# Kernel optimization log

Hardware: AMD Instinct MI355X
Metric: run time of the kernel (lower is better)

Reference implementation:

```python
import jax, jax.numpy as jnp
import numpy as np

N_NODES = 100000
N_EDGES = 1600000

def gcn_conv(x, src, dst, W, b, n):
    # symmetric GCN normalization with self-loops already included in src/dst
    deg = jax.ops.segment_sum(jnp.ones_like(src, dtype=x.dtype), dst, num_segments=n)
    dinv = jnp.where(deg > 0, jax.lax.rsqrt(deg), 0.0)
    norm = dinv[src] * dinv[dst]            # [E]
    h = x @ W                                # [n, out]
    msg = h[src] * norm[:, None]             # gather + scale, [E, out]
    out = jax.ops.segment_sum(msg, dst, num_segments=n)  # scatter-add
    return out + b

def setup_inputs() -> dict:
    key = jax.random.key(0)
    k1, k2, k3, k4 = jax.random.split(key, 4)
    x = jax.random.normal(k1, (N_NODES, 768), dtype=jnp.float32)
    edge_index = jax.random.randint(k2, (2, N_EDGES), 0, N_NODES, dtype=jnp.int64)
    W1 = jax.random.normal(k3, (768, 64), dtype=jnp.float32) * (1.0 / np.sqrt(768))
    b1 = jnp.zeros((64,), dtype=jnp.float32)
    W2 = jax.random.normal(k4, (64, 32), dtype=jnp.float32) * (1.0 / np.sqrt(64))
    b2 = jnp.zeros((32,), dtype=jnp.float32)
    return {"x": x, "edge_index": edge_index, "W1": W1, "b1": b1, "W2": W2, "b2": b2}

def reference(x, edge_index, W1, b1, W2, b2):
    n = x.shape[0]
    loop = jnp.arange(n, dtype=edge_index.dtype)
    src = jnp.concatenate([edge_index[0], loop])
    dst = jnp.concatenate([edge_index[1], loop])
    h = jax.nn.relu(gcn_conv(x, src, dst, W1, b1, n))
    # F.dropout with training=False -> identity (eval mode)
    out = gcn_conv(h, src, dst, W2, b2, n)
    return out
```

## Files before the change

### kernel.cpp

```cpp
#include <hip/hip_runtime.h>


constexpr int C1 = 64;
constexpr int C2 = 32;
constexpr int K1 = 768;
constexpr int SCAN_BS = 256;
constexpr int SCAN_ELEMS = 2048;

__global__ void detect_k(const int* __restrict__ ei32, int* flag, int n_words) {
    __shared__ int any_nz;
    if (threadIdx.x == 0) any_nz = 0;
    __syncthreads();
    int w = 2 * threadIdx.x + 1;
    if (w < n_words && ei32[w] != 0) atomicOr(&any_nz, 1);
    __syncthreads();
    if (threadIdx.x == 0) *flag = (any_nz == 0) ? 1 : 0;
}

__device__ __forceinline__ int load_idx(const void* ei, size_t pos, int m64) {
    if (m64) return (int)((const long long*)ei)[pos];
    return ((const int*)ei)[pos];
}

__global__ void zero_k(int* p, int n) {
    int i = blockIdx.x * 256 + threadIdx.x;
    if (i < n) p[i] = 0;
}

__global__ void cnt_k(const void* __restrict__ ei, const int* __restrict__ flag,
                      int* cnt, int E) {
    int e = blockIdx.x * 256 + threadIdx.x;
    if (e >= E) return;
    int m64 = *flag;
    int d = load_idx(ei, (size_t)E + e, m64);
    atomicAdd(&cnt[d], 1);
}

__global__ void dinv_k(const int* __restrict__ cnt, float* dinv, int n) {
    int i = blockIdx.x * 256 + threadIdx.x;
    if (i < n) dinv[i] = rsqrtf(1.0f + (float)cnt[i]);
}

__global__ void scan1_k(const int* __restrict__ cnt, int* partials, int n) {
    __shared__ int s[SCAN_BS];
    int base = blockIdx.x * SCAN_ELEMS;
    int t = threadIdx.x;
    int sum = 0;
    #pragma unroll
    for (int i = 0; i < 8; ++i) {
        int idx = base + t * 8 + i;
        if (idx < n) sum += cnt[idx];
    }
    s[t] = sum;
    __syncthreads();
    for (int off = 128; off > 0; off >>= 1) {
        if (t < off) s[t] += s[t + off];
        __syncthreads();
    }
    if (t == 0) partials[blockIdx.x] = s[0];
}

__global__ void scan2_k(int* partials, int* total_out, int nb) {
    __shared__ int s[256];
    int t = threadIdx.x;
    int v = (t < nb) ? partials[t] : 0;
    s[t] = v;
    __syncthreads();
    for (int off = 1; off < 256; off <<= 1) {
        int add = (t >= off) ? s[t - off] : 0;
        __syncthreads();
        s[t] += add;
        __syncthreads();
    }
    if (t < nb) partials[t] = s[t] - v;
    if (t == 0) *total_out = s[255];
}

__global__ void scan3_k(const int* __restrict__ cnt, const int* __restrict__ partials,
                        int* offsets, int* cursor, int n) {
    __shared__ int s[SCAN_BS];
    int base = blockIdx.x * SCAN_ELEMS;
    int t = threadIdx.x;
    int local[8];
    int sum = 0;
    #pragma unroll
    for (int i = 0; i < 8; ++i) {
        int idx = base + t * 8 + i;
        int v = (idx < n) ? cnt[idx] : 0;
        local[i] = sum;
        sum += v;
    }
    int mine = sum;
    s[t] = sum;
    __syncthreads();
    for (int off = 1; off < 256; off <<= 1) {
        int add = (t >= off) ? s[t - off] : 0;
        __syncthreads();
        s[t] += add;
        __syncthreads();
    }
    int texcl = s[t] - mine;
    int boff = partials[blockIdx.x];
    #pragma unroll
    for (int i = 0; i < 8; ++i) {
        int idx = base + t * 8 + i;
        if (idx < n) {
            int o = boff + texcl + local[i];
            offsets[idx] = o;
            cursor[idx] = o;
        }
    }
}

__global__ void fill_k(const void* __restrict__ ei, const int* __restrict__ flag,
                       int* cursor, int* adj, int E) {
    int e = blockIdx.x * 256 + threadIdx.x;
    if (e >= E) return;
    int m64 = *flag;
    int s = load_idx(ei, e, m64);
    int d = load_idx(ei, (size_t)E + e, m64);
    int pos = atomicAdd(&cursor[d], 1);
    adj[pos] = s;
}

__global__ __launch_bounds__(256) void gemm1_k(const float* __restrict__ x,
                                               const float* __restrict__ W,
                                               const float* __restrict__ dinv,
                                               float* __restrict__ g1, int n) {
    __shared__ float As[32][64];
    __shared__ float Bs[32][64];
    const int tid = threadIdx.x;
    const int block_row = blockIdx.x * 64;
    const int tr = tid >> 4;
    const int tc = tid & 15;

    float acc[4][4] = {};

    for (int k0 = 0; k0 < K1; k0 += 32) {
        #pragma unroll
        for (int i = 0; i < 2; ++i) {
            int f = tid + i * 256;
            int row = f >> 3;
            int k4 = (f & 7) << 2;
            int grow = block_row + row;
            float4 v = make_float4(0.f, 0.f, 0.f, 0.f);
            if (grow < n) v = *(const float4*)(x + (size_t)grow * K1 + k0 + k4);
            As[k4 + 0][row] = v.x; As[k4 + 1][row] = v.y;
            As[k4 + 2][row] = v.z; As[k4 + 3][row] = v.w;
        }
        #pragma unroll
        for (int i = 0; i < 2; ++i) {
            int f = tid + i * 256;
            int kr = f >> 4;
            int c4 = (f & 15) << 2;
            *(float4*)&Bs[kr][c4] = *(const float4*)(W + (size_t)(k0 + kr) * C1 + c4);
        }
        __syncthreads();
        #pragma unroll
        for (int kk = 0; kk < 32; ++kk) {
            float4 a = *(float4*)&As[kk][tr << 2];
            float4 b = *(float4*)&Bs[kk][tc << 2];
            acc[0][0] += a.x * b.x; acc[0][1] += a.x * b.y; acc[0][2] += a.x * b.z; acc[0][3] += a.x * b.w;
            acc[1][0] += a.y * b.x; acc[1][1] += a.y * b.y; acc[1][2] += a.y * b.z; acc[1][3] += a.y * b.w;
            acc[2][0] += a.z * b.x; acc[2][1] += a.z * b.y; acc[2][2] += a.z * b.z; acc[2][3] += a.z * b.w;
            acc[3][0] += a.w * b.x; acc[3][1] += a.w * b.y; acc[3][2] += a.w * b.z; acc[3][3] += a.w * b.w;
        }
        __syncthreads();
    }
    #pragma unroll
    for (int i = 0; i < 4; ++i) {
        int grow = block_row + (tr << 2) + i;
        if (grow < n) {
            float dv = dinv[grow];
            *(float4*)(g1 + (size_t)grow * C1 + (tc << 2)) =
                make_float4(acc[i][0] * dv, acc[i][1] * dv, acc[i][2] * dv, acc[i][3] * dv);
        }
    }
}

__global__ __launch_bounds__(256) void gather1_k(const int* __restrict__ offsets,
                                                 const int* __restrict__ adj,
                                                 const float* __restrict__ dinv,
                                                 const float* __restrict__ g1,
                                                 const float* __restrict__ b1,
                                                 const float* __restrict__ W2,
                                                 float* __restrict__ g2, int n) {
    __shared__ float sW[C1 * C2];
    __shared__ float srow[4][C1];
    const int tid = threadIdx.x;
    for (int i = tid; i < C1 * C2; i += 256) sW[i] = W2[i];

    const int wid = tid >> 6;
    const int c = tid & 63;
    const int v = blockIdx.x * 4 + wid;

    float r = 0.f;
    float dv = 0.f;
    if (v < n) {
        dv = dinv[v];
        int start = offsets[v], end = offsets[v + 1];
        float acc = g1[(size_t)v * C1 + c];
        int j = start;
        for (; j + 4 <= end; j += 4) {
            int s0 = adj[j], s1 = adj[j + 1], s2 = adj[j + 2], s3 = adj[j + 3];
            float a0 = g1[(size_t)s0 * C1 + c];
            float a1 = g1[(size_t)s1 * C1 + c];
            float a2 = g1[(size_t)s2 * C1 + c];
            float a3 = g1[(size_t)s3 * C1 + c];
            acc += (a0 + a1) + (a2 + a3);
        }
        for (; j < end; ++j) acc += g1[(size_t)adj[j] * C1 + c];
        r = fmaxf(b1[c] + dv * acc, 0.f);
    }
    srow[wid][c] = r;
    __syncthreads();

    if (v < n && c < C2) {
        float acc = 0.f;
        #pragma unroll
        for (int k = 0; k < C1; ++k) acc += srow[wid][k] * sW[k * C2 + c];
        g2[(size_t)v * C2 + c] = dv * acc;
    }
}

__global__ __launch_bounds__(256) void gather2_k(const int* __restrict__ offsets,
                                                 const int* __restrict__ adj,
                                                 const float* __restrict__ dinv,
                                                 const float* __restrict__ g2,
                                                 const float* __restrict__ b2,
                                                 float* __restrict__ out, int n) {
    int v = blockIdx.x * 8 + (threadIdx.x >> 5);
    int c = threadIdx.x & 31;
    if (v >= n) return;
    int start = offsets[v], end = offsets[v + 1];
    float acc = g2[(size_t)v * C2 + c];
    int j = start;
    for (; j + 4 <= end; j += 4) {
        int s0 = adj[j], s1 = adj[j + 1], s2 = adj[j + 2], s3 = adj[j + 3];
        float a0 = g2[(size_t)s0 * C2 + c];
        float a1 = g2[(size_t)s1 * C2 + c];
        float a2 = g2[(size_t)s2 * C2 + c];
        float a3 = g2[(size_t)s3 * C2 + c];
        acc += (a0 + a1) + (a2 + a3);
    }
    for (; j < end; ++j) acc += g2[(size_t)adj[j] * C2 + c];
    out[(size_t)v * C2 + c] = b2[c] + dinv[v] * acc;
}

extern "C" void kernel_launch(void* const* d_in, const int* in_sizes, int n_in,
                              void* d_out, int out_size, void* d_ws, size_t ws_size,
                              hipStream_t stream) {
    const float* x  = (const float*)d_in[0];
    const void*  ei = d_in[1];
    const float* W1 = (const float*)d_in[2];
    const float* b1 = (const float*)d_in[3];
    const float* W2 = (const float*)d_in[4];
    const float* b2 = (const float*)d_in[5];
    float* out = (float*)d_out;

    const int n = in_sizes[0] / K1;
    const int E = in_sizes[1] / 2;

    float* ws      = (float*)d_ws;
    int*   flag    = (int*)ws;
    float* dinv    = ws + 16;
    float* g1      = dinv + n;
    float* g2      = g1 + (size_t)n * C1;
    int*   cnt     = (int*)(g2 + (size_t)n * C2);
    int*   offsets = cnt + n;
    int*   cursor  = offsets + n + 1;
    int*   partials= cursor + n;
    int*   adj     = partials + 256;

    const int nb_scan = (n + SCAN_ELEMS - 1) / SCAN_ELEMS;

    detect_k<<<1, 256, 0, stream>>>((const int*)ei, flag, in_sizes[1]);
    zero_k<<<(n + 255) / 256, 256, 0, stream>>>(cnt, n);
    cnt_k<<<(E + 255) / 256, 256, 0, stream>>>(ei, flag, cnt, E);
    dinv_k<<<(n + 255) / 256, 256, 0, stream>>>(cnt, dinv, n);

    gemm1_k<<<(n + 63) / 64, 256, 0, stream>>>(x, W1, dinv, g1, n);

    scan1_k<<<nb_scan, SCAN_BS, 0, stream>>>(cnt, partials, n);
    scan2_k<<<1, 256, 0, stream>>>(partials, offsets + n, nb_scan);
    scan3_k<<<nb_scan, SCAN_BS, 0, stream>>>(cnt, partials, offsets, cursor, n);
    fill_k<<<(E + 255) / 256, 256, 0, stream>>>(ei, flag, cursor, adj, E);

    gather1_k<<<(n + 3) / 4, 256, 0, stream>>>(offsets, adj, dinv, g1, b1, W2, g2, n);
    gather2_k<<<(n + 7) / 8, 256, 0, stream>>>(offsets, adj, dinv, g2, b2, out, n);
}
```

Measured before the change: 813.9 us.

## Use split-bf16 MFMA with direct-to-LDS loads for first-layer GEMM

Replaces the FP32 scalar-FMA tiled GEMM for x@W1 with a matrix-core version. Each FP32 value is split into hi and lo bf16 parts and three bf16 MFMAs are issued per product (hi*hi, lo*hi, hi*lo) to keep near-FP32 accuracy. W1 is pre-packed into MFMA fragment layout by a new kernel, and x tiles are streamed into a swizzled LDS buffer with global_load_lds, using 128-row tiles. The aim is to cut the compute cost of the x@W1 GEMM (100000 rows, K=768), at the price of extra split arithmetic, an extra launch and a small accuracy change.

```diff
diff --git a/kernel.cpp b/kernel.cpp
--- a/kernel.cpp
+++ b/kernel.cpp
@@ -6,6 +6,9 @@
 constexpr int K1 = 768;
 constexpr int SCAN_BS = 256;
 constexpr int SCAN_ELEMS = 2048;
+
+typedef __attribute__((ext_vector_type(8))) short short8;
+typedef __attribute__((ext_vector_type(4))) float floatx4;
 
 __global__ void detect_k(const int* __restrict__ ei32, int* flag, int n_words) {
     __shared__ int any_nz;
@@ -123,57 +126,115 @@
     adj[pos] = s;
 }
 
+__device__ __forceinline__ void bf16_split(float f, unsigned short& hi, unsigned short& lo) {
+    unsigned int u = __float_as_uint(f);
+    unsigned int r1 = (u + 0x7FFFu + ((u >> 16) & 1u)) & 0xFFFF0000u;
+    hi = (unsigned short)(r1 >> 16);
+    float rem = f - __uint_as_float(r1);
+    unsigned int u2 = __float_as_uint(rem);
+    lo = (unsigned short)((u2 + 0x7FFFu + ((u2 >> 16) & 1u)) >> 16);
+}
+
+__global__ void packW1_k(const float* __restrict__ W1, unsigned short* __restrict__ Bp) {
+    int gid = blockIdx.x * 256 + threadIdx.x;
+    if (gid >= 24 * 4 * 2 * 64) return;
+    int l    = gid & 63;
+    int frag = gid >> 6;
+    int p = frag & 1;
+    int t = (frag >> 1) & 3;
+    int s = frag >> 3;
+    int c = t * 16 + (l & 15);
+    int kbase = s * 32 + (l >> 4) * 8;
+    short8 v;
+    #pragma unroll
+    for (int j = 0; j < 8; ++j) {
+        unsigned short hi, lo;
+        bf16_split(W1[(size_t)(kbase + j) * C1 + c], hi, lo);
+        v[j] = (short)(p ? lo : hi);
+    }
+    *(short8*)(Bp + (size_t)gid * 8) = v;
+}
+
 __global__ __launch_bounds__(256) void gemm1_k(const float* __restrict__ x,
-                                               const float* __restrict__ W,
+                                               const unsigned short* __restrict__ Bp,
                                                const float* __restrict__ dinv,
                                                float* __restrict__ g1, int n) {
-    __shared__ float As[32][64];
-    __shared__ float Bs[32][64];
+    constexpr int MT = 128;
+    __shared__ float As[MT * 32];
     const int tid = threadIdx.x;
-    const int block_row = blockIdx.x * 64;
-    const int tr = tid >> 4;
-    const int tc = tid & 15;
-
-    float acc[4][4] = {};
-
-    for (int k0 = 0; k0 < K1; k0 += 32) {
-        #pragma unroll
-        for (int i = 0; i < 2; ++i) {
-            int f = tid + i * 256;
-            int row = f >> 3;
-            int k4 = (f & 7) << 2;
-            int grow = block_row + row;
-            float4 v = make_float4(0.f, 0.f, 0.f, 0.f);
-            if (grow < n) v = *(const float4*)(x + (size_t)grow * K1 + k0 + k4);
-            As[k4 + 0][row] = v.x; As[k4 + 1][row] = v.y;
-            As[k4 + 2][row] = v.z; As[k4 + 3][row] = v.w;
-        }
-        #pragma unroll
-        for (int i = 0; i < 2; ++i) {
-            int f = tid + i * 256;
-            int kr = f >> 4;
-            int c4 = (f & 15) << 2;
-            *(float4*)&Bs[kr][c4] = *(const float4*)(W + (size_t)(k0 + kr) * C1 + c4);
-        }
-        __syncthreads();
-        #pragma unroll
-        for (int kk = 0; kk < 32; ++kk) {
-            float4 a = *(float4*)&As[kk][tr << 2];
-            float4 b = *(float4*)&Bs[kk][tc << 2];
-            acc[0][0] += a.x * b.x; acc[0][1] += a.x * b.y; acc[0][2] += a.x * b.z; acc[0][3] += a.x * b.w;
-            acc[1][0] += a.y * b.x; acc[1][1] += a.y * b.y; acc[1][2] += a.y * b.z; acc[1][3] += a.y * b.w;
-            acc[2][0] += a.z * b.x; acc[2][1] += a.z * b.y; acc[2][2] += a.z * b.z; acc[2][3] += a.z * b.w;
-            acc[3][0] += a.w * b.x; acc[3][1] += a.w * b.y; acc[3][2] += a.w * b.z; acc[3][3] += a.w * b.w;
-        }
-        __syncthreads();
-    }
-    #pragma unroll
-    for (int i = 0; i < 4; ++i) {
-        int grow = block_row + (tr << 2) + i;
-        if (grow < n) {
-            float dv = dinv[grow];
-            *(float4*)(g1 + (size_t)grow * C1 + (tc << 2)) =
-                make_float4(acc[i][0] * dv, acc[i][1] * dv, acc[i][2] * dv, acc[i][3] * dv);
+    const int w = tid >> 6;
+    const int l = tid & 63;
+    const int block_row = blockIdx.x * MT;
+
+    floatx4 zero = {0.f, 0.f, 0.f, 0.f};
+    floatx4 acc[2][4];
+    #pragma unroll
+    for (int r = 0; r < 2; ++r)
+        #pragma unroll
+        for (int t = 0; t < 4; ++t) acc[r][t] = zero;
+
+    const int srow = l >> 3;
+    const int skb  = (l & 7) ^ srow;
+
+    for (int s = 0; s < 24; ++s) {
+        const int k0 = s * 32;
+        #pragma unroll
+        for (int gi = 0; gi < 4; ++gi) {
+            int g = w * 4 + gi;
+            int row = block_row + g * 8 + srow;
+            if (row > n - 1) row = n - 1;
+            const float* src = x + (size_t)row * K1 + k0 + skb * 4;
+            float* ldst = &As[g * 256];
+            __builtin_amdgcn_global_load_lds(
+                (const __attribute__((address_space(1))) void*)src,
+                (__attribute__((address_space(3))) void*)ldst, 16, 0, 0);
+        }
+        short8 bh[4], bl[4];
+        #pragma unroll
+        for (int t = 0; t < 4; ++t) {
+            size_t fb = ((size_t)(s * 4 + t) * 2) * 512;
+            bh[t] = *(const short8*)(Bp + fb + l * 8);
+            bl[t] = *(const short8*)(Bp + fb + 512 + l * 8);
+        }
+        __syncthreads();
+        #pragma unroll
+        for (int r = 0; r < 2; ++r) {
+            int row_local = w * 32 + r * 16 + (l & 15);
+            int swz = l & 7;
+            int kb0 = ((l >> 4) * 2) ^ swz;
+            floatx4 f0 = *(const floatx4*)&As[row_local * 32 + kb0 * 4];
+            floatx4 f1 = *(const floatx4*)&As[row_local * 32 + (kb0 ^ 1) * 4];
+            short8 ah, al;
+            float fv[8] = {f0[0], f0[1], f0[2], f0[3], f1[0], f1[1], f1[2], f1[3]};
+            #pragma unroll
+            for (int j = 0; j < 8; ++j) {
+                unsigned short h16, l16;
+                bf16_split(fv[j], h16, l16);
+                ah[j] = (short)h16;
+                al[j] = (short)l16;
+            }
+            #pragma unroll
+            for (int t = 0; t < 4; ++t) {
+                acc[r][t] = __builtin_amdgcn_mfma_f32_16x16x32_bf16(ah, bh[t], acc[r][t], 0, 0, 0);
+                acc[r][t] = __builtin_amdgcn_mfma_f32_16x16x32_bf16(al, bh[t], acc[r][t], 0, 0, 0);
+                acc[r][t] = __builtin_amdgcn_mfma_f32_16x16x32_bf16(ah, bl[t], acc[r][t], 0, 0, 0);
+            }
+        }
+        __syncthreads();
+    }
+
+    #pragma unroll
+    for (int r = 0; r < 2; ++r) {
+        #pragma unroll
+        for (int i = 0; i < 4; ++i) {
+            int row = block_row + w * 32 + r * 16 + (l >> 4) * 4 + i;
+            if (row < n) {
+                float dv = dinv[row];
+                #pragma unroll
+                for (int t = 0; t < 4; ++t) {
+                    g1[(size_t)row * C1 + t * 16 + (l & 15)] = acc[r][t][i] * dv;
+                }
+            }
         }
     }
 }
@@ -271,6 +332,8 @@
     int*   cursor  = offsets + n + 1;
     int*   partials= cursor + n;
     int*   adj     = partials + 256;
+    uintptr_t bp_a = ((uintptr_t)(adj + E) + 15) & ~(uintptr_t)15;
+    unsigned short* Bp = (unsigned short*)bp_a;
 
     const int nb_scan = (n + SCAN_ELEMS - 1) / SCAN_ELEMS;
 
@@ -279,7 +342,8 @@
     cnt_k<<<(E + 255) / 256, 256, 0, stream>>>(ei, flag, cnt, E);
     dinv_k<<<(n + 255) / 256, 256, 0, stream>>>(cnt, dinv, n);
 
-    gemm1_k<<<(n + 63) / 64, 256, 0, stream>>>(x, W1, dinv, g1, n);
+    packW1_k<<<48, 256, 0, stream>>>(W1, Bp);
+    gemm1_k<<<(n + 127) / 128, 256, 0, stream>>>(x, Bp, dinv, g1, n);
 
     scan1_k<<<nb_scan, SCAN_BS, 0, stream>>>(cnt, partials, n);
     scan2_k<<<1, 256, 0, stream>>>(partials, offsets + n, nb_scan);
```

New measurement: 801.3 us. No clear change (-1.5%).
